# Optimization experiments

Hardware: AMD Instinct MI355X
Metric: run time of the kernel (lower is better)

The kernel has to match this reference:

```python
import jax, jax.numpy as jnp
import numpy as np

B, C, N, T = 8, 64, 170, 512
LEAK = 0.01
TEMP = 0.5


def _conv2d(x, w, b):
    # x: [B,C,N,Tp], w: [O,I,1,k] -> valid conv along time
    y = jax.lax.conv_general_dilated(x, w, (1, 1), 'VALID',
                                     dimension_numbers=('NCHW', 'OIHW', 'NCHW'))
    return y + b[None, :, None, None]


def _branch(x, w5, b5, w3, b3):
    # ReplicationPad2d((3,3,0,0)) -> Conv(1,5) -> LeakyReLU -> Conv(1,3) -> Tanh
    xp = jnp.pad(x, ((0, 0), (0, 0), (0, 0), (3, 3)), mode='edge')
    h = _conv2d(xp, w5, b5)
    h = jnp.where(h >= 0, h, LEAK * h)
    h = _conv2d(h, w3, b3)
    return jnp.tanh(h)


def _diff_gcn(x, adj, w, b):
    # Diffusion_GCN, support_len=1, order=1: concat([x, x@adj]) -> 1x1 conv
    x1 = jnp.einsum('bcnt,nm->bcmt', x, adj)
    h = jnp.concatenate([x, x1], axis=1)  # [B,2C,N,T]
    return jnp.einsum('bknt,ok->bont', h, w[:, :, 0, 0]) + b[None, :, None, None]


def _gumbel(k, shape, eps=1e-20):
    u = jax.random.uniform(k, shape, jnp.float32)
    return -jnp.log(-jnp.log(u + eps) + eps)


def _graph_gen(x, adj, g, ggw, ggb, fc0w, fc0b, fc1w, fc1b, fc2w, fc2b):
    h = _diff_gcn(x, adj, ggw, ggb)          # [B,C,N,T]
    h = h[-1].sum(-1).T                      # last batch elem, sum over T -> [N,C]
    h = jnp.tanh(h @ fc0w.T + fc0b)
    h = jnp.tanh(h @ fc1w.T + fc1b)
    h = jnp.tanh(h @ fc2w.T + fc2b)
    logp = jax.nn.log_softmax(h, axis=-1)
    y_soft = jax.nn.softmax((logp + g) / TEMP, axis=-1)
    y_hard = jax.nn.one_hot(jnp.argmax(y_soft, axis=-1), y_soft.shape[-1], dtype=y_soft.dtype)
    y = jax.lax.stop_gradient(y_hard - y_soft) + y_soft  # straight-through
    return y * (1.0 - jnp.eye(y.shape[0], dtype=y.dtype))  # zero diagonal


def _forward(x, nv1, nv2, a, c1w5, c1b5, c1w3, c1b3, c2w5, c2b5, c2w3, c2b3,
             c3w5, c3b5, c3w3, c3b3, c4w5, c4b5, c4w3, c4b3,
             ggw, ggb, fc0w, fc0b, fc1w, fc1b, fc2w, fc2b, dcw, dcb, gs):
    adj = jax.nn.softmax(jax.nn.relu(nv1 @ nv2), axis=1)
    xe, xo = x[..., ::2], x[..., 1::2]
    gg = (ggw, ggb, fc0w, fc0b, fc1w, fc1b, fc2w, fc2b)

    def step(xin, w5, b5, w3, b3, g):
        h = _branch(xin, w5, b5, w3, b3)
        la = _graph_gen(h, adj, g, *gg)
        dadj = la * a + adj * (1.0 - a)
        return h + _diff_gcn(h, dadj, dcw, dcb), dadj

    x1, dadj = step(xe, c1w5, c1b5, c1w3, c1b3, gs[0])
    d = xo * jnp.tanh(x1)
    x2, dadj = step(xo, c2w5, c2b5, c2w3, c2b3, gs[1])
    c = xe * jnp.tanh(x2)
    x3, dadj = step(c, c3w5, c3b5, c3w3, c3b3, gs[2])
    x_odd_update = d - x3
    x4, dadj = step(d, c4w5, c4b5, c4w3, c4b3, gs[3])
    x_even_update = c + x4
    return x_even_update, x_odd_update, dadj


def setup_inputs() -> dict:
    key = jax.random.key(0)
    ks = jax.random.split(key, 16)

    def rn(i, shape, s):
        return jax.random.normal(ks[i], shape, jnp.float32) * s

    inp = {'x': rn(0, (B, C, N, T), 1.0),
           'nv1': rn(1, (N, 10), 1.0),
           'nv2': rn(2, (10, N), 1.0),
           'a': jnp.array([0.5], jnp.float32)}
    i = 3
    for p in ('c1', 'c2', 'c3', 'c4'):
        inp[p + 'w5'] = rn(i, (C, C, 1, 5), 0.05); i += 1
        inp[p + 'b5'] = jnp.zeros((C,), jnp.float32)
        inp[p + 'w3'] = rn(i, (C, C, 1, 3), 0.05); i += 1
        inp[p + 'b3'] = jnp.zeros((C,), jnp.float32)
    inp['ggw'] = rn(i, (C, 2 * C, 1, 1), 0.08); i += 1
    inp['ggb'] = jnp.zeros((C,), jnp.float32)
    inp['fc0w'] = rn(i, (N, C), 0.1); i += 1
    inp['fc0b'] = jnp.zeros((N,), jnp.float32)
    inp['fc1w'] = rn(i, (2 * N, N), 0.06); i += 1
    inp['fc1b'] = jnp.zeros((2 * N,), jnp.float32)
    inp['fc2w'] = rn(i, (N, 2 * N), 0.05); i += 1
    inp['fc2b'] = jnp.zeros((N,), jnp.float32)
    inp['dcw'] = rn(i, (C, 2 * C, 1, 1), 0.08); i += 1
    inp['dcb'] = jnp.zeros((C,), jnp.float32)
    return inp


def reference(x, nv1, nv2, a, c1w5, c1b5, c1w3, c1b3, c2w5, c2b5, c2w3, c2b3,
              c3w5, c3b5, c3w3, c3b3, c4w5, c4b5, c4w3, c4b3,
              ggw, ggb, fc0w, fc0b, fc1w, fc1b, fc2w, fc2b, dcw, dcb):
    n = nv1.shape[0]
    gk = jax.random.split(jax.random.key(42), 4)
    gs = tuple(_gumbel(k, (n, n)) for k in gk)
    return _forward(x, nv1, nv2, a, c1w5, c1b5, c1w3, c1b3, c2w5, c2b5, c2w3, c2b3,
                    c3w5, c3b5, c3w3, c3b3, c4w5, c4b5, c4w3, c4b3,
                    ggw, ggb, fc0w, fc0b, fc1w, fc1b, fc2w, fc2b, dcw, dcb, gs)
```

## Files before the change

kernel.cpp:

```cpp
#include <hip/hip_runtime.h>
#include <hip/hip_bf16.h>
#include <cstdint>
#include <cstddef>

using bf16 = __hip_bfloat16;

static constexpr int BBATCH = 8, CCH = 64, NNODE = 170, TT = 256;
static constexpr size_t HSZ  = (size_t)BBATCH * CCH * NNODE * TT;
static constexpr size_t H7SZ = (size_t)CCH * NNODE * TT;
static constexpr int GN = NNODE * NNODE;

typedef __attribute__((ext_vector_type(8))) short short8v;
typedef __attribute__((ext_vector_type(4))) float f32x4;

__device__ __forceinline__ float b2f(bf16 v) { return __bfloat162float(v); }
__device__ __forceinline__ bf16  f2b(float v) { return __float2bfloat16(v); }

union BfU { bf16 h; unsigned short s; };
__device__ __forceinline__ unsigned short bfbits(float v) { BfU u; u.h = f2b(v); return u.s; }
__device__ __forceinline__ unsigned pack2(float a, float b) {
  return ((unsigned)bfbits(b) << 16) | bfbits(a);
}
__device__ __forceinline__ unsigned pks(short lo, short hi) {
  return ((unsigned)(unsigned short)hi << 16) | (unsigned short)lo;
}
__device__ __forceinline__ float shortbf(short s) { BfU u; u.s = (unsigned short)s; return b2f(u.h); }

__device__ __forceinline__ float tanhfast(float v) {
  float e = __expf(2.f * v);
  return 1.f - 2.f / (e + 1.f);
}

__device__ __forceinline__ unsigned rotl32(unsigned v, int d) { return (v << d) | (v >> (32 - d)); }

__device__ void threefry2x32(unsigned k0, unsigned k1, unsigned x0, unsigned x1,
                             unsigned& y0, unsigned& y1) {
  unsigned ks0 = k0, ks1 = k1, ks2 = k0 ^ k1 ^ 0x1BD11BDAu;
  x0 += ks0; x1 += ks1;
  const int ra[4] = {13, 15, 26, 6};
  const int rb[4] = {17, 29, 16, 24};
#pragma unroll
  for (int r = 0; r < 4; r++) { x0 += x1; x1 = rotl32(x1, ra[r]); x1 ^= x0; }
  x0 += ks1; x1 += ks2 + 1u;
#pragma unroll
  for (int r = 0; r < 4; r++) { x0 += x1; x1 = rotl32(x1, rb[r]); x1 ^= x0; }
  x0 += ks2; x1 += ks0 + 2u;
#pragma unroll
  for (int r = 0; r < 4; r++) { x0 += x1; x1 = rotl32(x1, ra[r]); x1 ^= x0; }
  x0 += ks0; x1 += ks1 + 3u;
#pragma unroll
  for (int r = 0; r < 4; r++) { x0 += x1; x1 = rotl32(x1, rb[r]); x1 ^= x0; }
  x0 += ks1; x1 += ks2 + 4u;
#pragma unroll
  for (int r = 0; r < 4; r++) { x0 += x1; x1 = rotl32(x1, ra[r]); x1 ^= x0; }
  x0 += ks2; x1 += ks0 + 5u;
  y0 = x0; y1 = x1;
}

struct SetupArgs {
  const float* w5[4]; const float* w3[4];
  float* wT5[4]; float* wT3[4];
  short* wp5[4]; short* wp3[4];
  const float* dcw; short* dcwP;
  const float* nv1; const float* nv2; float* adj;
  float* g;
};

__global__ __launch_bounds__(256) void k_setup(SetupArgs a) {
  const int blk = blockIdx.x;
  const int tid = threadIdx.x;
  __shared__ float red[256];

  if (blk < 170) {
    const int i = blk, j = tid;
    float val = 0.f, r = -1e30f;
    if (j < NNODE) {
      float acc = 0.f;
      for (int k = 0; k < 10; k++) acc += a.nv1[i*10+k] * a.nv2[k*NNODE+j];
      val = acc > 0.f ? acc : 0.f;
      r = val;
    }
    red[j] = r; __syncthreads();
    for (int s = 128; s; s >>= 1) { if (j < s) red[j] = fmaxf(red[j], red[j+s]); __syncthreads(); }
    float m = red[0]; __syncthreads();
    float e = (j < NNODE) ? expf(val - m) : 0.f;
    red[j] = e; __syncthreads();
    for (int s = 128; s; s >>= 1) { if (j < s) red[j] += red[j+s]; __syncthreads(); }
    if (j < NNODE) a.adj[i*NNODE+j] = e / red[0];
    return;
  }
  if (blk < 622) {
    int idx = (blk - 170) * 256 + tid;
    if (idx >= 4 * GN) return;
    int w = idx / GN, i = idx % GN;
    unsigned k0, k1, y0, y1;
    threefry2x32(0u, 42u, 0u, (unsigned)w, k0, k1);
    threefry2x32(k0, k1, 0u, (unsigned)i, y0, y1);
    unsigned bits = y0 ^ y1;
    unsigned fb = (bits >> 9) | 0x3f800000u;
    float u = __uint_as_float(fb) - 1.0f;
    a.g[idx] = -logf(-logf(u + 1e-20f) + 1e-20f);
    return;
  }
  if (blk < 942) {
    int gi = blk - 622, s = gi / 80;
    int idx = (gi - s*80) * 256 + tid;
    if (idx >= 20480) return;
    int oc = idx / 5, k = idx - oc * 5;
    int o = oc >> 6, c = oc & 63;
    a.wT5[s][(c*5 + k)*64 + o] = a.w5[s][idx];
    return;
  }
  if (blk < 1134) {
    int gi = blk - 942, s = gi / 48;
    int idx = (gi - s*48) * 256 + tid;
    if (idx >= 12288) return;
    int oc = idx / 3, k = idx - oc * 3;
    int o = oc >> 6, c = oc & 63;
    a.wT3[s][(c*3 + k)*64 + o] = a.w3[s][idx];
    return;
  }
  if (blk < 1454) {
    int gi = blk - 1134, s = gi / 80;
    int idx = (gi - s*80) * 256 + tid;
    if (idx >= 20480) return;
    int j = idx & 7, l = (idx >> 3) & 63, mi = (idx >> 9) & 3, ks = (idx >> 11) & 1, k = idx >> 12;
    int o = mi*16 + (l & 15);
    int c = ks*32 + (l >> 4)*8 + j;
    a.wp5[s][idx] = (short)bfbits(a.w5[s][(o*64 + c)*5 + k]);
    return;
  }
  if (blk < 1646) {
    int gi = blk - 1454, s = gi / 48;
    int idx = (gi - s*48) * 256 + tid;
    if (idx >= 12288) return;
    int j = idx & 7, l = (idx >> 3) & 63, mi = (idx >> 9) & 3, ks = (idx >> 11) & 1, k = idx >> 12;
    int o = mi*16 + (l & 15);
    int c = ks*32 + (l >> 4)*8 + j;
    a.wp3[s][idx] = (short)bfbits(a.w3[s][(o*64 + c)*3 + k]);
    return;
  }
  {
    int idx = (blk - 1646) * 256 + tid;
    if (idx >= 8192) return;
    int j = idx & 7, l = (idx >> 3) & 63, mi = (idx >> 9) & 3, kk = idx >> 11;
    int o = mi*16 + (l & 15);
    int c = kk*32 + (l >> 4)*8 + j;
    a.dcwP[idx] = (short)bfbits(a.dcw[o*128 + c]);
  }
}

__global__ __launch_bounds__(256) void k_packD(const float* __restrict__ dadj, short* __restrict__ out) {
  int idx = blockIdx.x * 256 + threadIdx.x;
  if (idx >= 33792) return;
  int j = idx & 7, l = (idx >> 3) & 63;
  int g = idx >> 9;
  int ks = g % 6, mi = g / 6;
  int m = mi*16 + (l & 15);
  int n = ks*32 + (l >> 4)*8 + j;
  float v = (m < NNODE && n < NNODE) ? dadj[n*NNODE + m] : 0.f;
  out[idx] = (short)bfbits(v);
}

__global__ __launch_bounds__(256) void k_branch(
    const float* __restrict__ src, int par,
    const float* __restrict__ wT5, const float* __restrict__ b5,
    const float* __restrict__ wT3, const float* __restrict__ b3,
    const short* __restrict__ wp5, const short* __restrict__ wp3,
    bf16* __restrict__ hout, float* __restrict__ h7f, float* __restrict__ Spart) {
  const int n = blockIdx.x, q = blockIdx.y, b = blockIdx.z;
  const int tid = threadIdx.x;
  const int l = tid & 63;
  const int w = __builtin_amdgcn_readfirstlane(tid >> 6);
  const int t0 = q * 64;
  __shared__ char lds[35840];

  if (b == 7) {
    float (*xs)[72]  = (float(*)[72])lds;
    float (*h1s)[68] = (float(*)[68])(lds + 18432);
    const int o = l;
    const int base = w * 16;
    const bool w3x = (w == 3);

    for (int i = tid; i < 64 * 70; i += 256) {
      int c = i / 70, pl = i - c * 70;
      int t = t0 + pl - 3; t = t < 0 ? 0 : (t > 255 ? 255 : t);
      size_t sb = ((size_t)7 * 64 + c) * NNODE + n;
      xs[c][pl] = (par >= 0) ? src[sb * 512 + 2 * t + par] : src[sb * 256 + t];
    }
    __syncthreads();

    {
      float acc[16];
#pragma unroll
      for (int tt = 0; tt < 16; tt++) acc[tt] = 0.f;
      float aH0 = 0.f, aH1 = 0.f;
      const float* wp = wT5 + o;
      for (int c = 0; c < 64; c++) {
        float xv[22];
        float4 v0 = *(const float4*)&xs[c][base + 0];
        float4 v1 = *(const float4*)&xs[c][base + 4];
        float4 v2 = *(const float4*)&xs[c][base + 8];
        float4 v3 = *(const float4*)&xs[c][base + 12];
        float4 v4 = *(const float4*)&xs[c][base + 16];
        xv[0]=v0.x; xv[1]=v0.y; xv[2]=v0.z; xv[3]=v0.w;
        xv[4]=v1.x; xv[5]=v1.y; xv[6]=v1.z; xv[7]=v1.w;
        xv[8]=v2.x; xv[9]=v2.y; xv[10]=v2.z; xv[11]=v2.w;
        xv[12]=v3.x; xv[13]=v3.y; xv[14]=v3.z; xv[15]=v3.w;
        xv[16]=v4.x; xv[17]=v4.y; xv[18]=v4.z; xv[19]=v4.w;
        if (w3x) { float2 vt = *(const float2*)&xs[c][68]; xv[20]=vt.x; xv[21]=vt.y; }
        float w0 = wp[0], w1 = wp[64], w2 = wp[128], w3_ = wp[192], w4 = wp[256];
        wp += 320;
#pragma unroll
        for (int tt = 0; tt < 16; tt++)
          acc[tt] += w0*xv[tt] + w1*xv[tt+1] + w2*xv[tt+2] + w3_*xv[tt+3] + w4*xv[tt+4];
        if (w3x) {
          aH0 += w0*xv[16] + w1*xv[17] + w2*xv[18] + w3_*xv[19] + w4*xv[20];
          aH1 += w0*xv[17] + w1*xv[18] + w2*xv[19] + w3_*xv[20] + w4*xv[21];
        }
      }
      float bias = b5[o];
#pragma unroll
      for (int tt = 0; tt < 16; tt++) {
        float v = acc[tt] + bias;
        h1s[o][base + tt] = v >= 0.f ? v : 0.01f * v;
      }
      if (w3x) {
        float u0 = aH0 + bias, u1 = aH1 + bias;
        h1s[o][64] = u0 >= 0.f ? u0 : 0.01f * u0;
        h1s[o][65] = u1 >= 0.f ? u1 : 0.01f * u1;
      }
    }
    __syncthreads();

    {
      float acc[16];
#pragma unroll
      for (int tt = 0; tt < 16; tt++) acc[tt] = 0.f;
      const float* wp = wT3 + o;
      for (int c = 0; c < 64; c++) {
        float hv[18];
        float4 v0 = *(const float4*)&h1s[c][base + 0];
        float4 v1 = *(const float4*)&h1s[c][base + 4];
        float4 v2 = *(const float4*)&h1s[c][base + 8];
        float4 v3 = *(const float4*)&h1s[c][base + 12];
        float4 v4 = *(const float4*)&h1s[c][base + 16];
        hv[0]=v0.x; hv[1]=v0.y; hv[2]=v0.z; hv[3]=v0.w;
        hv[4]=v1.x; hv[5]=v1.y; hv[6]=v1.z; hv[7]=v1.w;
        hv[8]=v2.x; hv[9]=v2.y; hv[10]=v2.z; hv[11]=v2.w;
        hv[12]=v3.x; hv[13]=v3.y; hv[14]=v3.z; hv[15]=v3.w;
        hv[16]=v4.x; hv[17]=v4.y;
        float w0 = wp[0], w1 = wp[64], w2 = wp[128];
        wp += 192;
#pragma unroll
        for (int tt = 0; tt < 16; tt++)
          acc[tt] += w0*hv[tt] + w1*hv[tt+1] + w2*hv[tt+2];
      }
      float bias = b3[o];
#pragma unroll
      for (int tt = 0; tt < 16; tt++) acc[tt] = tanhf(acc[tt] + bias);
      __syncthreads();
#pragma unroll
      for (int tt = 0; tt < 16; tt++) xs[o][base + tt] = acc[tt];
    }
    __syncthreads();

    {
      const int ro = tid >> 2, rq = tid & 3;
      float4 v0 = *(const float4*)&xs[ro][rq*16 + 0];
      float4 v1 = *(const float4*)&xs[ro][rq*16 + 4];
      float4 v2 = *(const float4*)&xs[ro][rq*16 + 8];
      float4 v3 = *(const float4*)&xs[ro][rq*16 + 12];
      float* dst = h7f + ((size_t)ro * NNODE + n) * TT + t0 + rq*16;
      *(float4*)&dst[0] = v0; *(float4*)&dst[4] = v1;
      *(float4*)&dst[8] = v2; *(float4*)&dst[12] = v3;
      float s = v0.x+v0.y+v0.z+v0.w + v1.x+v1.y+v1.z+v1.w
              + v2.x+v2.y+v2.z+v2.w + v3.x+v3.y+v3.z+v3.w;
      s += __shfl_xor(s, 1, 4);
      s += __shfl_xor(s, 2, 4);
      if (rq == 0) Spart[(q * 64 + ro) * NNODE + n] = s;
    }
    return;
  }

  const int mi = w;

  for (int it = 0; it < 16; it++) {
    int c = it * 4 + w;
    int t = t0 + l - 3; t = t < 0 ? 0 : (t > 255 ? 255 : t);
    size_t sb = ((size_t)b * 64 + c) * NNODE + n;
    float v = (par >= 0) ? src[sb * 512 + 2 * t + par] : src[sb * 256 + t];
    *(short*)(lds + l*128 + ((2*c) ^ ((l & 7) << 4))) = (short)bfbits(v);
  }
  for (int i = tid; i < 6 * 64; i += 256) {
    int tr = 64 + (i >> 6);
    int c = i & 63;
    int t = t0 + tr - 3; if (t > 255) t = 255;
    size_t sb = ((size_t)b * 64 + c) * NNODE + n;
    float v = (par >= 0) ? src[sb * 512 + 2 * t + par] : src[sb * 256 + t];
    *(short*)(lds + tr*128 + ((2*c) ^ ((tr & 7) << 4))) = (short)bfbits(v);
  }
  __syncthreads();

  f32x4 acc[5];
#pragma unroll
  for (int i = 0; i < 5; i++) acc[i] = (f32x4){0.f, 0.f, 0.f, 0.f};
  for (int k = 0; k < 5; k++) {
#pragma unroll
    for (int ks = 0; ks < 2; ks++) {
      short8v af = *(const short8v*)(wp5 + (size_t)((((k*2 + ks)*4 + mi)*64 + l) * 8));
      const int c0 = ks*32 + (l >> 4)*8;
#pragma unroll
      for (int ni = 0; ni < 5; ni++) {
        int tr = ni*16 + (l & 15) + k;
        short8v bf = *(const short8v*)(lds + tr*128 + ((2*c0) ^ ((tr & 7) << 4)));
        acc[ni] = __builtin_amdgcn_mfma_f32_16x16x32_bf16(af, bf, acc[ni], 0, 0, 0);
      }
    }
  }
  {
    const int o0 = mi*16 + ((l >> 4) << 2);
    float4 bv = *(const float4*)&b5[o0];
    float bb[4] = {bv.x, bv.y, bv.z, bv.w};
#pragma unroll
    for (int ni = 0; ni < 4; ni++) {
      int tr = ni*16 + (l & 15);
      float v[4];
#pragma unroll
      for (int r = 0; r < 4; r++) {
        float u = acc[ni][r] + bb[r];
        v[r] = u >= 0.f ? u : 0.01f * u;
      }
      int colb = (2*o0) ^ ((tr & 7) << 4);
      *(uint2*)(lds + 10752 + tr*128 + colb) = make_uint2(pack2(v[0], v[1]), pack2(v[2], v[3]));
    }
    if ((l & 15) < 2) {
      int tr = 64 + (l & 15);
      float v[4];
#pragma unroll
      for (int r = 0; r < 4; r++) {
        float u = acc[4][r] + bb[r];
        v[r] = u >= 0.f ? u : 0.01f * u;
      }
      int colb = (2*o0) ^ ((tr & 7) << 4);
      *(uint2*)(lds + 10752 + tr*128 + colb) = make_uint2(pack2(v[0], v[1]), pack2(v[2], v[3]));
    }
  }
  __syncthreads();

  f32x4 acc3[4];
#pragma unroll
  for (int i = 0; i < 4; i++) acc3[i] = (f32x4){0.f, 0.f, 0.f, 0.f};
  for (int k = 0; k < 3; k++) {
#pragma unroll
    for (int ks = 0; ks < 2; ks++) {
      short8v af = *(const short8v*)(wp3 + (size_t)((((k*2 + ks)*4 + mi)*64 + l) * 8));
      const int c0 = ks*32 + (l >> 4)*8;
#pragma unroll
      for (int ni = 0; ni < 4; ni++) {
        int tr = ni*16 + (l & 15) + k;
        short8v bf = *(const short8v*)(lds + 10752 + tr*128 + ((2*c0) ^ ((tr & 7) << 4)));
        acc3[ni] = __builtin_amdgcn_mfma_f32_16x16x32_bf16(af, bf, acc3[ni], 0, 0, 0);
      }
    }
  }
  {
    const int o0 = mi*16 + ((l >> 4) << 2);
    float4 bv = *(const float4*)&b3[o0];
    float bb[4] = {bv.x, bv.y, bv.z, bv.w};
#pragma unroll
    for (int ni = 0; ni < 4; ni++) {
      int t = ni*16 + (l & 15);
#pragma unroll
      for (int r = 0; r < 4; r++) {
        float v = tanhfast(acc3[ni][r] + bb[r]);
        *(short*)(lds + (o0 + r)*144 + t*2) = (short)bfbits(v);
      }
    }
  }
  __syncthreads();

  {
    const int ro = tid >> 2, rq = tid & 3;
    uint4 p0 = *(const uint4*)(lds + ro*144 + rq*32);
    uint4 p1 = *(const uint4*)(lds + ro*144 + rq*32 + 16);
    bf16* dst = hout + (((size_t)b * 64 + ro) * NNODE + n) * TT + t0 + rq*16;
    *(uint4*)&dst[0] = p0;
    *(uint4*)&dst[8] = p1;
  }
}

__global__ __launch_bounds__(256) void k_sredT(const float* __restrict__ Spart, float* __restrict__ ST) {
  int idx = blockIdx.x * 256 + threadIdx.x;
  if (idx >= CCH * NNODE) return;
  int nn = idx >> 6, c = idx & 63;
  float acc = 0.f;
#pragma unroll
  for (int qq = 0; qq < 4; qq++) acc += Spart[(qq * 64 + c) * NNODE + nn];
  ST[idx] = acc;
}

__global__ __launch_bounds__(256) void k_gg(const float* __restrict__ ST, const float* __restrict__ adj,
    const float* __restrict__ ggw, const float* __restrict__ ggb,
    const float* __restrict__ fc0w, const float* __restrict__ fc0b,
    const float* __restrict__ fc1w, const float* __restrict__ fc1b,
    const float* __restrict__ fc2w, const float* __restrict__ fc2b,
    const float* __restrict__ g, const float* __restrict__ a_in,
    float* __restrict__ dadj, float* __restrict__ out_tail) {
  const int i = blockIdx.x;
  const int tid = threadIdx.x;
  __shared__ float s1[64], sc[64], h0r[64];
  __shared__ float a1r[NNODE];
  __shared__ float a2r[340];
  __shared__ float vred[256];
  __shared__ int ired[256];
  if (tid < 64) {
    const int c = tid;
    float acc = 0.f;
    for (int nn = 0; nn < NNODE; nn++) acc += ST[nn*64 + c] * adj[nn*NNODE + i];
    s1[c] = acc;
    sc[c] = ST[i*64 + c];
  }
  __syncthreads();
  if (tid < 64) {
    const int o = tid;
    float acc = 256.f * ggb[o];
    for (int c = 0; c < 64; c++)
      acc += ggw[o*128 + c] * sc[c] + ggw[o*128 + 64 + c] * s1[c];
    h0r[o] = acc;
  }
  __syncthreads();
  if (tid < NNODE) {
    float acc = fc0b[tid];
    for (int o = 0; o < 64; o++) acc += h0r[o] * fc0w[tid*64 + o];
    a1r[tid] = tanhf(acc);
  }
  __syncthreads();
  for (int j = tid; j < 340; j += 256) {
    float acc = fc1b[j];
    for (int k = 0; k < NNODE; k++) acc += a1r[k] * fc1w[j*NNODE + k];
    a2r[j] = tanhf(acc);
  }
  __syncthreads();
  float v = -1e30f;
  if (tid < NNODE) {
    float acc = fc2b[tid];
    for (int k = 0; k < 340; k++) acc += a2r[k] * fc2w[tid*340 + k];
    v = tanhf(acc) + g[i*NNODE + tid];
  }
  vred[tid] = v; ired[tid] = tid;
  __syncthreads();
  for (int s = 128; s; s >>= 1) {
    if (tid < s) {
      if (vred[tid+s] > vred[tid]) { vred[tid] = vred[tid+s]; ired[tid] = ired[tid+s]; }
    }
    __syncthreads();
  }
  int jmax = ired[0];
  float a = a_in[0];
  if (tid < NNODE) {
    float la = (tid == jmax && jmax != i) ? 1.f : 0.f;
    float dv = la * a + adj[i*NNODE + tid] * (1.f - a);
    dadj[i*NNODE + tid] = dv;
    if (out_tail) out_tail[i*NNODE + tid] = dv;
  }
}

__global__ __launch_bounds__(256) void k_hA_m(const bf16* __restrict__ h, const short* __restrict__ dP,
                                              bf16* __restrict__ hA) {
  const int bc = blockIdx.x, tq = blockIdx.y;
  const int tid = threadIdx.x;
  const int l = tid & 63;
  const int w = __builtin_amdgcn_readfirstlane(tid >> 6);
  const int t0 = tq * 64;
  __shared__ char lds[25600];

  const bf16* hp = h + (size_t)bc * NNODE * TT;
  for (int i = tid; i < 170*64; i += 256) {
    int n = i >> 6, t = i & 63;
    *(short*)(lds + t*400 + ((2*n) ^ ((t & 7) << 4))) = *(const short*)&hp[(size_t)n * TT + t0 + t];
  }
  for (int i = tid; i < 22*64; i += 256) {
    int n = 170 + (i >> 6), t = i & 63;
    *(short*)(lds + t*400 + ((2*n) ^ ((t & 7) << 4))) = 0;
  }
  __syncthreads();

  f32x4 acc[11];
#pragma unroll
  for (int i = 0; i < 11; i++) acc[i] = (f32x4){0.f, 0.f, 0.f, 0.f};
  const int tr = w*16 + (l & 15);
#pragma unroll
  for (int ks = 0; ks < 6; ks++) {
    const int n0 = ks*32 + (l >> 4)*8;
    short8v bf = *(const short8v*)(lds + tr*400 + ((2*n0) ^ ((tr & 7) << 4)));
#pragma unroll
    for (int mi = 0; mi < 11; mi++) {
      short8v af = *(const short8v*)(dP + (size_t)(((mi*6 + ks)*64 + l) * 8));
      acc[mi] = __builtin_amdgcn_mfma_f32_16x16x32_bf16(af, bf, acc[mi], 0, 0, 0);
    }
  }

  bf16* dst = hA + (size_t)bc * NNODE * TT + t0 + w*16 + (l & 15);
#pragma unroll
  for (int mi = 0; mi < 11; mi++) {
#pragma unroll
    for (int r = 0; r < 4; r++) {
      int m = mi*16 + ((l >> 4) << 2) + r;
      if (m < NNODE) dst[(size_t)m * TT] = f2b(acc[mi][r]);
    }
  }
}

__global__ __launch_bounds__(256) void k_hA7(const float* __restrict__ h7f,
                                             const float* __restrict__ dadj,
                                             float* __restrict__ hA7f) {
  const int c = blockIdx.x, tq = blockIdx.y;
  const int t0 = tq * 32;
  const int tid = threadIdx.x;
  const int lane = tid & 63;
  const int w = __builtin_amdgcn_readfirstlane(tid >> 6);
  __shared__ float hs[170][33];
  for (int i = tid; i < 170*32; i += 256) {
    int nn = i >> 5, tl = i & 31;
    hs[nn][tl] = h7f[((size_t)c * NNODE + nn) * TT + t0 + tl];
  }
  __syncthreads();
  float acc0[8], acc1[8], acc2[8];
#pragma unroll
  for (int tt = 0; tt < 8; tt++) { acc0[tt] = 0.f; acc1[tt] = 0.f; acc2[tt] = 0.f; }
  const int toff = w * 8;
  for (int nn = 0; nn < NNODE; nn++) {
    float hv[8];
#pragma unroll
    for (int tt = 0; tt < 8; tt++) hv[tt] = hs[nn][toff + tt];
    const float* dr = &dadj[nn * NNODE];
    float w0 = dr[lane];
    float w1 = dr[64 + lane];
    float w2 = (lane < 42) ? dr[128 + lane] : 0.f;
#pragma unroll
    for (int tt = 0; tt < 8; tt++) {
      acc0[tt] += w0 * hv[tt];
      acc1[tt] += w1 * hv[tt];
      acc2[tt] += w2 * hv[tt];
    }
  }
  __syncthreads();
#pragma unroll
  for (int tt = 0; tt < 8; tt++) {
    hs[lane][toff + tt] = acc0[tt];
    hs[64 + lane][toff + tt] = acc1[tt];
    if (lane < 42) hs[128 + lane][toff + tt] = acc2[tt];
  }
  __syncthreads();
  if (tid < NNODE) {
    float* dst = hA7f + ((size_t)c * NNODE + tid) * TT + t0;
#pragma unroll
    for (int j = 0; j < 8; j++)
      *(float4*)&dst[j*4] = make_float4(hs[tid][j*4], hs[tid][j*4+1], hs[tid][j*4+2], hs[tid][j*4+3]);
  }
}

__global__ __launch_bounds__(256) void k_mix_m(const bf16* __restrict__ h, const bf16* __restrict__ hA,
                                               const short* __restrict__ dcwP, const float* __restrict__ dcb,
                                               const float* __restrict__ x,
                                               float* __restrict__ oute, float* __restrict__ outo, int epi) {
  const int n = blockIdx.x, b = blockIdx.y, tq = blockIdx.z;
  const int tid = threadIdx.x;
  const int l = tid & 63;
  const int mi = __builtin_amdgcn_readfirstlane(tid >> 6);
  const int t0 = tq * 64;
  __shared__ char lds[16384];

#pragma unroll
  for (int it = 0; it < 8; it++) {
    int c0 = it * 8 + mi * 2;
    size_t off = (((size_t)b * 64 + c0) * NNODE + n) * TT + t0 + l;
    size_t off1 = off + (size_t)NNODE * TT;
    *(unsigned*)(lds + l*256 + ((2*c0) ^ ((l & 7) << 4))) =
        pks(*(const short*)&h[off], *(const short*)&h[off1]);
    *(unsigned*)(lds + l*256 + ((2*(64 + c0)) ^ ((l & 7) << 4))) =
        pks(*(const short*)&hA[off], *(const short*)&hA[off1]);
  }
  __syncthreads();

  f32x4 acc[4];
#pragma unroll
  for (int i = 0; i < 4; i++) acc[i] = (f32x4){0.f, 0.f, 0.f, 0.f};
#pragma unroll
  for (int kk = 0; kk < 4; kk++) {
    short8v af = *(const short8v*)(dcwP + (size_t)(((kk*4 + mi)*64 + l) * 8));
    const int c0 = kk*32 + (l >> 4)*8;
#pragma unroll
    for (int ni = 0; ni < 4; ni++) {
      int tr = ni*16 + (l & 15);
      short8v bf = *(const short8v*)(lds + tr*256 + ((2*c0) ^ ((tr & 7) << 4)));
      acc[ni] = __builtin_amdgcn_mfma_f32_16x16x32_bf16(af, bf, acc[ni], 0, 0, 0);
    }
  }

  const int o0 = mi*16 + ((l >> 4) << 2);
  float dcb4[4];
#pragma unroll
  for (int r = 0; r < 4; r++) dcb4[r] = dcb[o0 + r];
#pragma unroll
  for (int ni = 0; ni < 4; ni++) {
    int t = ni*16 + (l & 15);
#pragma unroll
    for (int r = 0; r < 4; r++) {
      const int o = o0 + r;
      float hres = shortbf(*(const short*)(lds + t*256 + ((2*o) ^ ((t & 7) << 4))));
      float v = acc[ni][r] + hres + dcb4[r];
      size_t oidx = (((size_t)b * 64 + o) * NNODE + n) * TT + t0 + t;
      if (epi == 1) {
        outo[oidx] = x[(((size_t)b * 64 + o) * NNODE + n) * 512 + 2*(t0 + t) + 1] * tanhfast(v);
      } else if (epi == 2) {
        oute[oidx] = x[(((size_t)b * 64 + o) * NNODE + n) * 512 + 2*(t0 + t)] * tanhfast(v);
      } else if (epi == 3) {
        outo[oidx] -= v;
      } else {
        oute[oidx] += v;
      }
    }
  }
}

__global__ __launch_bounds__(256) void k_mix7(const float* __restrict__ h7f, const float* __restrict__ hA7f,
                                              const float* __restrict__ dcw, const float* __restrict__ dcb,
                                              const float* __restrict__ x,
                                              float* __restrict__ oute, float* __restrict__ outo, int epi) {
  const int n = blockIdx.x, tq = blockIdx.y;
  const int tid = threadIdx.x;
  const int lane = tid & 63;
  const int w = __builtin_amdgcn_readfirstlane(tid >> 6);
  const int t = tq * 64 + lane;
  __shared__ float wTs[128][64];
  __shared__ float hsf[64][64];
  __shared__ float hasf[64][64];
  for (int i = tid; i < 8192; i += 256) {
    int o_ = i & 63, cf_ = i >> 6;
    wTs[cf_][o_] = dcw[o_*128 + cf_];
  }
  for (int i = tid; i < 4096; i += 256) {
    int c = i >> 6, tl = i & 63;
    size_t off = ((size_t)c * NNODE + n) * TT + tq * 64 + tl;
    hsf[c][tl] = h7f[off];
    hasf[c][tl] = hA7f[off];
  }
  __syncthreads();
  const int o0 = w * 16;
  float acc[16];
#pragma unroll
  for (int oo = 0; oo < 16; oo++) acc[oo] = 0.f;
  for (int cc = 0; cc < 64; cc++) {
    float hv = hsf[cc][lane];
    float hav = hasf[cc][lane];
    float4 wh0 = *(const float4*)&wTs[cc][o0 + 0];
    float4 wh1 = *(const float4*)&wTs[cc][o0 + 4];
    float4 wh2 = *(const float4*)&wTs[cc][o0 + 8];
    float4 wh3 = *(const float4*)&wTs[cc][o0 + 12];
    float4 wa0 = *(const float4*)&wTs[64 + cc][o0 + 0];
    float4 wa1 = *(const float4*)&wTs[64 + cc][o0 + 4];
    float4 wa2 = *(const float4*)&wTs[64 + cc][o0 + 8];
    float4 wa3 = *(const float4*)&wTs[64 + cc][o0 + 12];
    acc[0]  += wh0.x*hv + wa0.x*hav;  acc[1]  += wh0.y*hv + wa0.y*hav;
    acc[2]  += wh0.z*hv + wa0.z*hav;  acc[3]  += wh0.w*hv + wa0.w*hav;
    acc[4]  += wh1.x*hv + wa1.x*hav;  acc[5]  += wh1.y*hv + wa1.y*hav;
    acc[6]  += wh1.z*hv + wa1.z*hav;  acc[7]  += wh1.w*hv + wa1.w*hav;
    acc[8]  += wh2.x*hv + wa2.x*hav;  acc[9]  += wh2.y*hv + wa2.y*hav;
    acc[10] += wh2.z*hv + wa2.z*hav;  acc[11] += wh2.w*hv + wa2.w*hav;
    acc[12] += wh3.x*hv + wa3.x*hav;  acc[13] += wh3.y*hv + wa3.y*hav;
    acc[14] += wh3.z*hv + wa3.z*hav;  acc[15] += wh3.w*hv + wa3.w*hav;
  }
#pragma unroll
  for (int oo = 0; oo < 16; oo++) {
    const int o = o0 + oo;
    float v = acc[oo] + hsf[o][lane] + dcb[o];
    size_t oidx = (((size_t)7 * 64 + o) * NNODE + n) * TT + t;
    if (epi == 1) {
      outo[oidx] = x[(((size_t)7 * 64 + o) * NNODE + n) * 512 + 2*t + 1] * tanhf(v);
    } else if (epi == 2) {
      oute[oidx] = x[(((size_t)7 * 64 + o) * NNODE + n) * 512 + 2*t] * tanhf(v);
    } else if (epi == 3) {
      outo[oidx] -= v;
    } else {
      oute[oidx] += v;
    }
  }
}

extern "C" void kernel_launch(void* const* d_in, const int* in_sizes, int n_in,
                              void* d_out, int out_size, void* d_ws, size_t ws_size,
                              hipStream_t stream) {
  const float* x    = (const float*)d_in[0];
  const float* nv1  = (const float*)d_in[1];
  const float* nv2  = (const float*)d_in[2];
  const float* a_in = (const float*)d_in[3];
  const float *w5[4], *b5[4], *w3[4], *b3[4];
  for (int s = 0; s < 4; s++) {
    w5[s] = (const float*)d_in[4 + 4*s];
    b5[s] = (const float*)d_in[5 + 4*s];
    w3[s] = (const float*)d_in[6 + 4*s];
    b3[s] = (const float*)d_in[7 + 4*s];
  }
  const float* ggw  = (const float*)d_in[20];
  const float* ggb  = (const float*)d_in[21];
  const float* fc0w = (const float*)d_in[22];
  const float* fc0b = (const float*)d_in[23];
  const float* fc1w = (const float*)d_in[24];
  const float* fc1b = (const float*)d_in[25];
  const float* fc2w = (const float*)d_in[26];
  const float* fc2b = (const float*)d_in[27];
  const float* dcw  = (const float*)d_in[28];
  const float* dcb  = (const float*)d_in[29];

  char* p = (char*)d_ws;
  size_t used = 0;
  auto alloc = [&](size_t bytes) -> char* {
    char* r = p + used;
    used += (bytes + 255) & ~(size_t)255;
    return r;
  };
  float* adjW   = (float*)alloc(GN*4);
  float* dadjW  = (float*)alloc(GN*4);
  float* gW     = (float*)alloc(4*GN*4);
  float* STa    = (float*)alloc(CCH*NNODE*4);
  float* STb    = (float*)alloc(CCH*NNODE*4);
  float* Spart  = (float*)alloc(4*CCH*NNODE*4);
  float* wT5[4]; float* wT3[4];
  short* wp5[4]; short* wp3[4];
  for (int s = 0; s < 4; s++) {
    wT5[s] = (float*)alloc(64*64*5*4);
    wT3[s] = (float*)alloc(64*64*3*4);
    wp5[s] = (short*)alloc(20480*2);
    wp3[s] = (short*)alloc(12288*2);
  }
  short* dcwP   = (short*)alloc(8192*2);
  short* dadjP  = (short*)alloc(33792*2);
  bf16* H1      = (bf16*)alloc(HSZ*2);
  bf16* H2      = (bf16*)alloc(HSZ*2);
  bf16* HA      = (bf16*)alloc(HSZ*2);
  float* h7fA   = (float*)alloc(H7SZ*4);
  float* h7fB   = (float*)alloc(H7SZ*4);
  float* hA7f   = (float*)alloc(H7SZ*4);
  if (used > ws_size) return;

  float* oute = (float*)d_out;
  float* outo = oute + HSZ;
  float* tail = oute + 2*HSZ;

  dim3 bgrid(NNODE, 4, BBATCH);
  dim3 agrid(448, 4);
  dim3 a7grid(64, 8);
  dim3 mgrid(NNODE, 7, 4);
  dim3 m7grid(NNODE, 4);

  SetupArgs sa;
  for (int s = 0; s < 4; s++) {
    sa.w5[s] = w5[s]; sa.w3[s] = w3[s];
    sa.wT5[s] = wT5[s]; sa.wT3[s] = wT3[s];
    sa.wp5[s] = wp5[s]; sa.wp3[s] = wp3[s];
  }
  sa.dcw = dcw; sa.dcwP = dcwP;
  sa.nv1 = nv1; sa.nv2 = nv2; sa.adj = adjW;
  sa.g = gW;
  k_setup<<<1678, 256, 0, stream>>>(sa);

  auto graph_pipe = [&](float* ST, const float* gstep, float* tailp) {
    k_sredT<<<43, 256, 0, stream>>>(Spart, ST);
    k_gg<<<NNODE, 256, 0, stream>>>(ST, adjW, ggw, ggb, fc0w, fc0b, fc1w, fc1b,
                                    fc2w, fc2b, gstep, a_in, dadjW, tailp);
    k_packD<<<132, 256, 0, stream>>>(dadjW, dadjP);
  };
  auto hA_all = [&](bf16* Hb, float* h7f) {
    k_hA_m<<<agrid, 256, 0, stream>>>(Hb, dadjP, HA);
    k_hA7<<<a7grid, 256, 0, stream>>>(h7f, dadjW, hA7f);
  };
  auto mix_all = [&](bf16* Hb, float* h7f, int epi) {
    k_mix_m<<<mgrid, 256, 0, stream>>>(Hb, HA, dcwP, dcb, x, oute, outo, epi);
    k_mix7<<<m7grid, 256, 0, stream>>>(h7f, hA7f, dcw, dcb, x, oute, outo, epi);
  };

  k_branch<<<bgrid, 256, 0, stream>>>(x, 0, wT5[0], b5[0], wT3[0], b3[0], wp5[0], wp3[0], H1, h7fA, Spart);
  graph_pipe(STa, gW, nullptr);
  hA_all(H1, h7fA);
  mix_all(H1, h7fA, 1);

  k_branch<<<bgrid, 256, 0, stream>>>(x, 1, wT5[1], b5[1], wT3[1], b3[1], wp5[1], wp3[1], H1, h7fA, Spart);
  graph_pipe(STa, gW + GN, nullptr);
  hA_all(H1, h7fA);
  mix_all(H1, h7fA, 2);

  k_branch<<<bgrid, 256, 0, stream>>>(oute, -1, wT5[2], b5[2], wT3[2], b3[2], wp5[2], wp3[2], H1, h7fA, Spart);
  k_sredT<<<43, 256, 0, stream>>>(Spart, STa);
  k_branch<<<bgrid, 256, 0, stream>>>(outo, -1, wT5[3], b5[3], wT3[3], b3[3], wp5[3], wp3[3], H2, h7fB, Spart);
  k_sredT<<<43, 256, 0, stream>>>(Spart, STb);

  k_gg<<<NNODE, 256, 0, stream>>>(STa, adjW, ggw, ggb, fc0w, fc0b, fc1w, fc1b,
                                  fc2w, fc2b, gW + 2*GN, a_in, dadjW, nullptr);
  k_packD<<<132, 256, 0, stream>>>(dadjW, dadjP);
  hA_all(H1, h7fA);
  mix_all(H1, h7fA, 3);

  k_gg<<<NNODE, 256, 0, stream>>>(STb, adjW, ggw, ggb, fc0w, fc0b, fc1w, fc1b,
                                  fc2w, fc2b, gW + 3*GN, a_in, dadjW, tail);
  k_packD<<<132, 256, 0, stream>>>(dadjW, dadjP);
  hA_all(H2, h7fB);
  mix_all(H2, h7fB, 4);

  (void)in_sizes; (void)n_in; (void)out_size;
}
```

Baseline: 1.458 ms.

## Batch the two independent SCINet steps into merged double-grid kernel launches

The even and odd interaction steps, which are data-independent, now run together in each phase. Every kernel (branch, S reduction, graph generation, pack, diffusion and mix) takes a step index from the grid and selects per-step pointers, so the step count drops from four sequential pipelines to two phases with doubled grids. The aim is to cut launch count and serialization, and to fill the GPU better in the smaller graph and pack kernels. It needs extra workspace for second HA and hA7 buffers, and falls back to sequential launches when the workspace is too small.

```diff
diff --git a/kernel.cpp b/kernel.cpp
--- a/kernel.cpp
+++ b/kernel.cpp
@@ -150,30 +150,17 @@
   }
 }
 
-__global__ __launch_bounds__(256) void k_packD(const float* __restrict__ dadj, short* __restrict__ out) {
-  int idx = blockIdx.x * 256 + threadIdx.x;
-  if (idx >= 33792) return;
-  int j = idx & 7, l = (idx >> 3) & 63;
-  int g = idx >> 9;
-  int ks = g % 6, mi = g / 6;
-  int m = mi*16 + (l & 15);
-  int n = ks*32 + (l >> 4)*8 + j;
-  float v = (m < NNODE && n < NNODE) ? dadj[n*NNODE + m] : 0.f;
-  out[idx] = (short)bfbits(v);
-}
-
-__global__ __launch_bounds__(256) void k_branch(
+__device__ void branch_body(int n, int q, int b,
     const float* __restrict__ src, int par,
     const float* __restrict__ wT5, const float* __restrict__ b5,
     const float* __restrict__ wT3, const float* __restrict__ b3,
     const short* __restrict__ wp5, const short* __restrict__ wp3,
-    bf16* __restrict__ hout, float* __restrict__ h7f, float* __restrict__ Spart) {
-  const int n = blockIdx.x, q = blockIdx.y, b = blockIdx.z;
+    bf16* __restrict__ hout, float* __restrict__ h7f, float* __restrict__ Spart,
+    char* lds) {
   const int tid = threadIdx.x;
   const int l = tid & 63;
   const int w = __builtin_amdgcn_readfirstlane(tid >> 6);
   const int t0 = q * 64;
-  __shared__ char lds[35840];
 
   if (b == 7) {
     float (*xs)[72]  = (float(*)[72])lds;
@@ -390,24 +377,54 @@
   }
 }
 
-__global__ __launch_bounds__(256) void k_sredT(const float* __restrict__ Spart, float* __restrict__ ST) {
-  int idx = blockIdx.x * 256 + threadIdx.x;
+__global__ __launch_bounds__(256) void k_branch2(
+    const float* src0, const float* src1, int par0, int par1,
+    const float* wT5_0, const float* wT5_1, const float* b5_0, const float* b5_1,
+    const float* wT3_0, const float* wT3_1, const float* b3_0, const float* b3_1,
+    const short* wp5_0, const short* wp5_1, const short* wp3_0, const short* wp3_1,
+    bf16* hout0, bf16* hout1, float* h7f0, float* h7f1, float* Sp0, float* Sp1) {
+  __shared__ char lds[35840];
+  const int step = blockIdx.z >> 3;
+  const int b = blockIdx.z & 7;
+  branch_body(blockIdx.x, blockIdx.y, b,
+              step ? src1 : src0, step ? par1 : par0,
+              step ? wT5_1 : wT5_0, step ? b5_1 : b5_0,
+              step ? wT3_1 : wT3_0, step ? b3_1 : b3_0,
+              step ? wp5_1 : wp5_0, step ? wp3_1 : wp3_0,
+              step ? hout1 : hout0, step ? h7f1 : h7f0, step ? Sp1 : Sp0, lds);
+}
+
+__global__ __launch_bounds__(256) void k_sredT2(const float* __restrict__ Sp0, const float* __restrict__ Sp1,
+                                                float* __restrict__ ST0, float* __restrict__ ST1) {
+  int gidx = blockIdx.x * 256 + threadIdx.x;
+  int step = gidx >= CCH*NNODE;
+  int idx = gidx - step * CCH*NNODE;
   if (idx >= CCH * NNODE) return;
+  const float* Sp = step ? Sp1 : Sp0;
+  float* ST = step ? ST1 : ST0;
   int nn = idx >> 6, c = idx & 63;
   float acc = 0.f;
 #pragma unroll
-  for (int qq = 0; qq < 4; qq++) acc += Spart[(qq * 64 + c) * NNODE + nn];
+  for (int qq = 0; qq < 4; qq++) acc += Sp[(qq * 64 + c) * NNODE + nn];
   ST[idx] = acc;
 }
 
-__global__ __launch_bounds__(256) void k_gg(const float* __restrict__ ST, const float* __restrict__ adj,
+__global__ __launch_bounds__(256) void k_gg2(const float* __restrict__ ST0, const float* __restrict__ ST1,
+    const float* __restrict__ adj,
     const float* __restrict__ ggw, const float* __restrict__ ggb,
     const float* __restrict__ fc0w, const float* __restrict__ fc0b,
     const float* __restrict__ fc1w, const float* __restrict__ fc1b,
     const float* __restrict__ fc2w, const float* __restrict__ fc2b,
-    const float* __restrict__ g, const float* __restrict__ a_in,
-    float* __restrict__ dadj, float* __restrict__ out_tail) {
+    const float* __restrict__ g0, const float* __restrict__ g1,
+    const float* __restrict__ a_in,
+    float* __restrict__ dadj0, float* __restrict__ dadj1,
+    float* __restrict__ tail0, float* __restrict__ tail1) {
   const int i = blockIdx.x;
+  const int step = blockIdx.y;
+  const float* ST = step ? ST1 : ST0;
+  const float* g = step ? g1 : g0;
+  float* dadj = step ? dadj1 : dadj0;
+  float* out_tail = step ? tail1 : tail0;
   const int tid = threadIdx.x;
   __shared__ float s1[64], sc[64], h0r[64];
   __shared__ float a1r[NNODE];
@@ -466,8 +483,29 @@
   }
 }
 
-__global__ __launch_bounds__(256) void k_hA_m(const bf16* __restrict__ h, const short* __restrict__ dP,
-                                              bf16* __restrict__ hA) {
+__global__ __launch_bounds__(256) void k_packD2(const float* __restrict__ dadj0, const float* __restrict__ dadj1,
+                                                short* __restrict__ out0, short* __restrict__ out1) {
+  int gidx = blockIdx.x * 256 + threadIdx.x;
+  int step = gidx >= 33792;
+  int idx = gidx - step * 33792;
+  if (idx >= 33792) return;
+  const float* dadj = step ? dadj1 : dadj0;
+  short* out = step ? out1 : out0;
+  int j = idx & 7, l = (idx >> 3) & 63;
+  int g = idx >> 9;
+  int ks = g % 6, mi = g / 6;
+  int m = mi*16 + (l & 15);
+  int n = ks*32 + (l >> 4)*8 + j;
+  float v = (m < NNODE && n < NNODE) ? dadj[n*NNODE + m] : 0.f;
+  out[idx] = (short)bfbits(v);
+}
+
+__global__ __launch_bounds__(256) void k_hA_m2(const bf16* __restrict__ h0, const short* __restrict__ dP0, bf16* __restrict__ hA0,
+                                               const bf16* __restrict__ h1, const short* __restrict__ dP1, bf16* __restrict__ hA1) {
+  const int step = blockIdx.z;
+  const bf16* h = step ? h1 : h0;
+  const short* dP = step ? dP1 : dP0;
+  bf16* hA = step ? hA1 : hA0;
   const int bc = blockIdx.x, tq = blockIdx.y;
   const int tid = threadIdx.x;
   const int l = tid & 63;
@@ -512,9 +550,12 @@
   }
 }
 
-__global__ __launch_bounds__(256) void k_hA7(const float* __restrict__ h7f,
-                                             const float* __restrict__ dadj,
-                                             float* __restrict__ hA7f) {
+__global__ __launch_bounds__(256) void k_hA7_2(const float* __restrict__ h7f0, const float* __restrict__ dadj0, float* __restrict__ hA7f0,
+                                               const float* __restrict__ h7f1, const float* __restrict__ dadj1, float* __restrict__ hA7f1) {
+  const int step = blockIdx.z;
+  const float* h7f = step ? h7f1 : h7f0;
+  const float* dadj = step ? dadj1 : dadj0;
+  float* hA7f = step ? hA7f1 : hA7f0;
   const int c = blockIdx.x, tq = blockIdx.y;
   const int t0 = tq * 32;
   const int tid = threadIdx.x;
@@ -561,11 +602,17 @@
   }
 }
 
-__global__ __launch_bounds__(256) void k_mix_m(const bf16* __restrict__ h, const bf16* __restrict__ hA,
-                                               const short* __restrict__ dcwP, const float* __restrict__ dcb,
-                                               const float* __restrict__ x,
-                                               float* __restrict__ oute, float* __restrict__ outo, int epi) {
-  const int n = blockIdx.x, b = blockIdx.y, tq = blockIdx.z;
+__global__ __launch_bounds__(256) void k_mix_m2(const bf16* __restrict__ h0, const bf16* __restrict__ hA0,
+                                                const bf16* __restrict__ h1, const bf16* __restrict__ hA1,
+                                                const short* __restrict__ dcwP, const float* __restrict__ dcb,
+                                                const float* __restrict__ x,
+                                                float* __restrict__ oute, float* __restrict__ outo, int epiBase) {
+  const int n = blockIdx.x, tq = blockIdx.z;
+  const int b = blockIdx.y % 7;
+  const int step = blockIdx.y / 7;
+  const bf16* h = step ? h1 : h0;
+  const bf16* hA = step ? hA1 : hA0;
+  const int epi = epiBase + step;
   const int tid = threadIdx.x;
   const int l = tid & 63;
   const int mi = __builtin_amdgcn_readfirstlane(tid >> 6);
@@ -625,11 +672,17 @@
   }
 }
 
-__global__ __launch_bounds__(256) void k_mix7(const float* __restrict__ h7f, const float* __restrict__ hA7f,
-                                              const float* __restrict__ dcw, const float* __restrict__ dcb,
-                                              const float* __restrict__ x,
-                                              float* __restrict__ oute, float* __restrict__ outo, int epi) {
-  const int n = blockIdx.x, tq = blockIdx.y;
+__global__ __launch_bounds__(256) void k_mix7_2(const float* __restrict__ h7f0, const float* __restrict__ hA7f0,
+                                                const float* __restrict__ h7f1, const float* __restrict__ hA7f1,
+                                                const float* __restrict__ dcw, const float* __restrict__ dcb,
+                                                const float* __restrict__ x,
+                                                float* __restrict__ oute, float* __restrict__ outo, int epiBase) {
+  const int n = blockIdx.x;
+  const int tq = blockIdx.y & 3;
+  const int step = blockIdx.y >> 2;
+  const float* h7f = step ? h7f1 : h7f0;
+  const float* hA7f = step ? hA7f1 : hA7f0;
+  const int epi = epiBase + step;
   const int tid = threadIdx.x;
   const int lane = tid & 63;
   const int w = __builtin_amdgcn_readfirstlane(tid >> 6);
@@ -722,11 +775,13 @@
     return r;
   };
   float* adjW   = (float*)alloc(GN*4);
-  float* dadjW  = (float*)alloc(GN*4);
+  float* dadjA  = (float*)alloc(GN*4);
+  float* dadjB  = (float*)alloc(GN*4);
   float* gW     = (float*)alloc(4*GN*4);
   float* STa    = (float*)alloc(CCH*NNODE*4);
   float* STb    = (float*)alloc(CCH*NNODE*4);
-  float* Spart  = (float*)alloc(4*CCH*NNODE*4);
+  float* SpA    = (float*)alloc(4*CCH*NNODE*4);
+  float* SpB    = (float*)alloc(4*CCH*NNODE*4);
   float* wT5[4]; float* wT3[4];
   short* wp5[4]; short* wp3[4];
   for (int s = 0; s < 4; s++) {
@@ -736,24 +791,31 @@
     wp3[s] = (short*)alloc(12288*2);
   }
   short* dcwP   = (short*)alloc(8192*2);
-  short* dadjP  = (short*)alloc(33792*2);
+  short* dPA    = (short*)alloc(33792*2);
+  short* dPB    = (short*)alloc(33792*2);
   bf16* H1      = (bf16*)alloc(HSZ*2);
   bf16* H2      = (bf16*)alloc(HSZ*2);
-  bf16* HA      = (bf16*)alloc(HSZ*2);
+  bf16* HAa     = (bf16*)alloc(HSZ*2);
   float* h7fA   = (float*)alloc(H7SZ*4);
   float* h7fB   = (float*)alloc(H7SZ*4);
-  float* hA7f   = (float*)alloc(H7SZ*4);
+  float* hA7fA  = (float*)alloc(H7SZ*4);
   if (used > ws_size) return;
+
+  bf16* HAb; float* hA7fB; bool merged;
+  {
+    size_t need = used + ((HSZ*2 + 255) & ~(size_t)255) + ((H7SZ*4 + 255) & ~(size_t)255);
+    if (need <= ws_size) {
+      HAb   = (bf16*)alloc(HSZ*2);
+      hA7fB = (float*)alloc(H7SZ*4);
+      merged = true;
+    } else {
+      HAb = HAa; hA7fB = hA7fA; merged = false;
+    }
+  }
 
   float* oute = (float*)d_out;
   float* outo = oute + HSZ;
   float* tail = oute + 2*HSZ;
-
-  dim3 bgrid(NNODE, 4, BBATCH);
-  dim3 agrid(448, 4);
-  dim3 a7grid(64, 8);
-  dim3 mgrid(NNODE, 7, 4);
-  dim3 m7grid(NNODE, 4);
 
   SetupArgs sa;
   for (int s = 0; s < 4; s++) {
@@ -766,47 +828,40 @@
   sa.g = gW;
   k_setup<<<1678, 256, 0, stream>>>(sa);
 
-  auto graph_pipe = [&](float* ST, const float* gstep, float* tailp) {
-    k_sredT<<<43, 256, 0, stream>>>(Spart, ST);
-    k_gg<<<NNODE, 256, 0, stream>>>(ST, adjW, ggw, ggb, fc0w, fc0b, fc1w, fc1b,
-                                    fc2w, fc2b, gstep, a_in, dadjW, tailp);
-    k_packD<<<132, 256, 0, stream>>>(dadjW, dadjP);
+  dim3 bgrid2(NNODE, 4, 16);
+
+  auto phase = [&](const float* srcA, const float* srcB, int parA, int parB,
+                   int sA, int sB, const float* gA, const float* gB,
+                   float* tailB, int epiBase) {
+    k_branch2<<<bgrid2, 256, 0, stream>>>(srcA, srcB, parA, parB,
+        wT5[sA], wT5[sB], b5[sA], b5[sB], wT3[sA], wT3[sB], b3[sA], b3[sB],
+        wp5[sA], wp5[sB], wp3[sA], wp3[sB],
+        H1, H2, h7fA, h7fB, SpA, SpB);
+    k_sredT2<<<86, 256, 0, stream>>>(SpA, SpB, STa, STb);
+    k_gg2<<<dim3(NNODE, 2), 256, 0, stream>>>(STa, STb, adjW, ggw, ggb,
+        fc0w, fc0b, fc1w, fc1b, fc2w, fc2b, gA, gB, a_in,
+        dadjA, dadjB, nullptr, tailB);
+    k_packD2<<<264, 256, 0, stream>>>(dadjA, dadjB, dPA, dPB);
+    if (merged) {
+      k_hA_m2<<<dim3(448, 4, 2), 256, 0, stream>>>(H1, dPA, HAa, H2, dPB, HAb);
+      k_hA7_2<<<dim3(64, 8, 2), 256, 0, stream>>>(h7fA, dadjA, hA7fA, h7fB, dadjB, hA7fB);
+      k_mix_m2<<<dim3(NNODE, 14, 4), 256, 0, stream>>>(H1, HAa, H2, HAb, dcwP, dcb, x, oute, outo, epiBase);
+      k_mix7_2<<<dim3(NNODE, 8), 256, 0, stream>>>(h7fA, hA7fA, h7fB, hA7fB, dcw, dcb, x, oute, outo, epiBase);
+    } else {
+      k_hA_m2<<<dim3(448, 4, 1), 256, 0, stream>>>(H1, dPA, HAa, H1, dPA, HAa);
+      k_hA7_2<<<dim3(64, 8, 1), 256, 0, stream>>>(h7fA, dadjA, hA7fA, h7fA, dadjA, hA7fA);
+      k_mix_m2<<<dim3(NNODE, 7, 4), 256, 0, stream>>>(H1, HAa, H1, HAa, dcwP, dcb, x, oute, outo, epiBase);
+      k_mix7_2<<<dim3(NNODE, 4), 256, 0, stream>>>(h7fA, hA7fA, h7fA, hA7fA, dcw, dcb, x, oute, outo, epiBase);
+      k_hA_m2<<<dim3(448, 4, 1), 256, 0, stream>>>(H2, dPB, HAa, H2, dPB, HAa);
+      k_hA7_2<<<dim3(64, 8, 1), 256, 0, stream>>>(h7fB, dadjB, hA7fA, h7fB, dadjB, hA7fA);
+      k_mix_m2<<<dim3(NNODE, 7, 4), 256, 0, stream>>>(H2, HAa, H2, HAa, dcwP, dcb, x, oute, outo, epiBase + 1);
+      k_mix7_2<<<dim3(NNODE, 4), 256, 0, stream>>>(h7fB, hA7fA, h7fB, hA7fA, dcw, dcb, x, oute, outo, epiBase + 1);
+    }
   };
-  auto hA_all = [&](bf16* Hb, float* h7f) {
-    k_hA_m<<<agrid, 256, 0, stream>>>(Hb, dadjP, HA);
-    k_hA7<<<a7grid, 256, 0, stream>>>(h7f, dadjW, hA7f);
-  };
-  auto mix_all = [&](bf16* Hb, float* h7f, int epi) {
-    k_mix_m<<<mgrid, 256, 0, stream>>>(Hb, HA, dcwP, dcb, x, oute, outo, epi);
-    k_mix7<<<m7grid, 256, 0, stream>>>(h7f, hA7f, dcw, dcb, x, oute, outo, epi);
-  };
-
-  k_branch<<<bgrid, 256, 0, stream>>>(x, 0, wT5[0], b5[0], wT3[0], b3[0], wp5[0], wp3[0], H1, h7fA, Spart);
-  graph_pipe(STa, gW, nullptr);
-  hA_all(H1, h7fA);
-  mix_all(H1, h7fA, 1);
-
-  k_branch<<<bgrid, 256, 0, stream>>>(x, 1, wT5[1], b5[1], wT3[1], b3[1], wp5[1], wp3[1], H1, h7fA, Spart);
-  graph_pipe(STa, gW + GN, nullptr);
-  hA_all(H1, h7fA);
-  mix_all(H1, h7fA, 2);
-
-  k_branch<<<bgrid, 256, 0, stream>>>(oute, -1, wT5[2], b5[2], wT3[2], b3[2], wp5[2], wp3[2], H1, h7fA, Spart);
-  k_sredT<<<43, 256, 0, stream>>>(Spart, STa);
-  k_branch<<<bgrid, 256, 0, stream>>>(outo, -1, wT5[3], b5[3], wT3[3], b3[3], wp5[3], wp3[3], H2, h7fB, Spart);
-  k_sredT<<<43, 256, 0, stream>>>(Spart, STb);
-
-  k_gg<<<NNODE, 256, 0, stream>>>(STa, adjW, ggw, ggb, fc0w, fc0b, fc1w, fc1b,
-                                  fc2w, fc2b, gW + 2*GN, a_in, dadjW, nullptr);
-  k_packD<<<132, 256, 0, stream>>>(dadjW, dadjP);
-  hA_all(H1, h7fA);
-  mix_all(H1, h7fA, 3);
-
-  k_gg<<<NNODE, 256, 0, stream>>>(STb, adjW, ggw, ggb, fc0w, fc0b, fc1w, fc1b,
-                                  fc2w, fc2b, gW + 3*GN, a_in, dadjW, tail);
-  k_packD<<<132, 256, 0, stream>>>(dadjW, dadjP);
-  hA_all(H2, h7fB);
-  mix_all(H2, h7fB, 4);
+
+  phase(x, x, 0, 1, 0, 1, gW, gW + GN, nullptr, 1);
+
+  phase(oute, outo, -1, -1, 2, 3, gW + 2*GN, gW + 3*GN, tail, 3);
 
   (void)in_sizes; (void)n_in; (void)out_size;
 }
```

Result: faster. 1.222 ms (-16.2%).
